# Performance work log

Measured on AMD Instinct MI355X. Metric: run time of the kernel, lower is better.

## Reference

```python
import jax, jax.numpy as jnp
import numpy as np

C_A = 768; C_S = 384; C_Z = 128; H = 16; D = C_A // H
B = 1; N = 4096; NQ = 32; NK = 128; NB = N // NQ
EPS = 1e-5


def _ln(x):
    # layernorm without learned affine (affine applied by caller where present)
    m = jnp.mean(x, axis=-1, keepdims=True)
    v = jnp.mean((x - m) ** 2, axis=-1, keepdims=True)
    return (x - m) * jax.lax.rsqrt(v + EPS)


def setup_inputs() -> dict:
    key = jax.random.key(0)
    ks = jax.random.split(key, 16)
    w = lambda k, shp: jax.random.normal(k, shp, dtype=jnp.float32) * 0.02
    return dict(
        a=jax.random.normal(ks[0], (B, N, C_A), jnp.float32),
        s=jax.random.normal(ks[1], (B, N, C_S), jnp.float32),
        z=jax.random.normal(ks[2], (B, NB, NQ, NK, C_Z), jnp.float32),
        adaln_gamma_s=jnp.ones((C_S,), jnp.float32),
        adaln_ws=w(ks[3], (C_S, C_A)),
        adaln_bs=jnp.zeros((C_A,), jnp.float32),
        adaln_wskip=w(ks[4], (C_S, C_A)),
        lnz_gamma=jnp.ones((C_Z,), jnp.float32),
        wz=w(ks[5], (C_Z, H)),
        wq=w(ks[6], (C_A, C_A)), bq=jnp.zeros((C_A,), jnp.float32),
        wk=w(ks[7], (C_A, C_A)),
        wv=w(ks[8], (C_A, C_A)),
        wg=w(ks[9], (C_A, C_A)), bg=jnp.ones((C_A,), jnp.float32),
        wo=w(ks[10], (C_A, C_A)), bo=jnp.zeros((C_A,), jnp.float32),
        w_last=w(ks[11], (C_S, C_A)),
        b_last=jnp.full((C_A,), -2.0, jnp.float32),  # biasinit = -2.0
        n_queries=NQ, n_keys=NK,
    )


def _forward(a, s, z, adaln_gamma_s, adaln_ws, adaln_bs, adaln_wskip,
             lnz_gamma, wz, wq, bq, wk, wv, wg, bg, wo, bo,
             w_last, b_last, n_queries, n_keys):
    Bq, Nq, _ = a.shape
    nb = Nq // n_queries
    # AdaptiveLayerNorm (AF3 Alg 26): a <- sigmoid(Lin(s_ln)) * LN(a) + LinNoBias(s_ln)
    s_ln = _ln(s) * adaln_gamma_s
    a_ln = jax.nn.sigmoid(s_ln @ adaln_ws + adaln_bs) * _ln(a) + s_ln @ adaln_wskip
    # pair bias: LN(z) (no offset) -> per-head bias, permuted to [B,H,nb,nq,nk]
    bias = (_ln(z) * lnz_gamma) @ wz                    # [B, nb, nq, nk, H]
    bias = jnp.transpose(bias, (0, 4, 1, 2, 3))          # [B, H, nb, nq, nk]
    # projections (q has bias; k/v no bias)
    q = (a_ln @ wq + bq).reshape(Bq, nb, n_queries, H, D)
    k = (a_ln @ wk).reshape(Bq, Nq, H, D)
    v = (a_ln @ wv).reshape(Bq, Nq, H, D)
    # local window: query block w covers [w*nq, (w+1)*nq); keys are nk centered on it
    start = jnp.arange(nb) * n_queries + n_queries // 2 - n_keys // 2
    kidx = start[:, None] + jnp.arange(n_keys)[None, :]  # [nb, nk]
    valid = (kidx >= 0) & (kidx < Nq)
    kidx = jnp.clip(kidx, 0, Nq - 1)
    k_loc = k[:, kidx]                                    # [B, nb, nk, H, D]
    v_loc = v[:, kidx]
    scale = 1.0 / float(np.sqrt(D))
    scores = jnp.einsum('bwqhd,bwkhd->bhwqk', q, k_loc) * scale + bias
    scores = jnp.where(valid[None, None, :, None, :], scores, -1e9)
    p = jax.nn.softmax(scores, axis=-1)
    o = jnp.einsum('bhwqk,bwkhd->bwqhd', p, v_loc).reshape(Bq, Nq, C_A)
    # gating, output projection, final sigmoid gate from raw s
    o = (jax.nn.sigmoid(a_ln @ wg + bg) * o) @ wo + bo
    return jax.nn.sigmoid(s @ w_last + b_last) * o


def reference(a, s, z, adaln_gamma_s, adaln_ws, adaln_bs, adaln_wskip,
              lnz_gamma, wz, wq, bq, wk, wv, wg, bg, wo, bo,
              w_last, b_last, n_queries, n_keys):
    return _forward(a, s, z, adaln_gamma_s, adaln_ws, adaln_bs, adaln_wskip,
                    lnz_gamma, wz, wq, bq, wk, wv, wg, bg, wo, bo,
                    w_last, b_last, n_queries, n_keys)
```

## Files before the change

### kernel.cpp

```cpp
#include <hip/hip_runtime.h>
#include <hip/hip_bf16.h>
#include <math.h>

#define N_TOK 4096
#define CA 768
#define CS 384
#define CZ 128
#define NHEAD 16
#define DH 48
#define NQW 32
#define NKW 128
#define NBLK 128
#define VT_W 4224

typedef __attribute__((ext_vector_type(8))) short short8;
typedef __attribute__((ext_vector_type(4))) float float4v;
typedef __attribute__((ext_vector_type(4))) unsigned short ushort4v;

__device__ __forceinline__ float sigmoidf_(float x){ return 1.0f/(1.0f+__expf(-x)); }

__device__ __forceinline__ unsigned short f2bf(float x){
  unsigned u = __float_as_uint(x);
  unsigned r = (u + 0x7FFFu + ((u>>16)&1u)) >> 16;
  return (unsigned short)r;
}
__device__ __forceinline__ float bf2f(unsigned short b){
  return __uint_as_float(((unsigned)b)<<16);
}
__device__ __forceinline__ short8 cvt8(const float* xv){
  union { short8 v; unsigned short u[8]; } H;
  #pragma unroll
  for (int j=0;j<8;j++) H.u[j] = f2bf(xv[j]);
  return H.v;
}
__device__ __forceinline__ short8 cvt8pk(const float* x){
  union { short8 v; unsigned u32[4]; } H;
  #pragma unroll
  for (int i=0;i<4;i++)
    asm("v_cvt_pk_bf16_f32 %0, %1, %2" : "=v"(H.u32[i]) : "v"(x[2*i]), "v"(x[2*i+1]));
  return H.v;
}

__device__ __forceinline__ void gload_lds16(const void* gsrc, void* ldst){
  __builtin_amdgcn_global_load_lds(
    (const __attribute__((address_space(1))) void*)gsrc,
    (__attribute__((address_space(3))) void*)ldst, 16, 0, 0);
}

__device__ __forceinline__ int xcd_swz(int wg, int nwg){
  int cpx = nwg >> 3;
  return (wg & 7)*cpx + (wg >> 3);
}

__global__ __launch_bounds__(256) void prep_kernel(
  const float* __restrict__ s, const float* __restrict__ adaln_gamma,
  unsigned short* __restrict__ s_ln_h, unsigned short* __restrict__ s_h,
  const float* __restrict__ a, float* __restrict__ a_n,
  const float* __restrict__ ws, const float* __restrict__ wskip,
  const float* __restrict__ wq, const float* __restrict__ wk,
  const float* __restrict__ wv, const float* __restrict__ wg,
  const float* __restrict__ wo, const float* __restrict__ wlast,
  unsigned short* __restrict__ Wt1, unsigned short* __restrict__ Wt2,
  unsigned short* __restrict__ Wt3, unsigned short* __restrict__ Wt4,
  const float* __restrict__ bq, const float* __restrict__ bg,
  float* __restrict__ biasq)
{
  __shared__ float tile[64][65];
  int bid = blockIdx.x;
  int tid = threadIdx.x;

  if (bid < 1024){
    int wave = tid>>6, lane = tid&63;
    int row = bid*4 + wave;
    const float* x = s + (size_t)row*CS;
    float v[6]; float sum=0.f, sq=0.f;
    #pragma unroll
    for (int i=0;i<6;i++){ v[i]=x[lane+64*i]; sum+=v[i]; sq+=v[i]*v[i]; }
    #pragma unroll
    for (int off=32; off; off>>=1){ sum+=__shfl_xor(sum,off); sq+=__shfl_xor(sq,off); }
    float m = sum*(1.f/CS);
    float var = sq*(1.f/CS)-m*m;
    float rs = rsqrtf(var+1e-5f);
    #pragma unroll
    for (int i=0;i<6;i++){
      int c = lane+64*i;
      s_ln_h[(size_t)row*CS+c] = f2bf((v[i]-m)*rs*adaln_gamma[c]);
      s_h[(size_t)row*CS+c]    = f2bf(v[i]);
    }
    return;
  }
  bid -= 1024;

  if (bid < 1024){
    int wave = tid>>6, lane = tid&63;
    int row = bid*4 + wave;
    const float* x = a + (size_t)row*CA;
    float v[12]; float sum=0.f, sq=0.f;
    #pragma unroll
    for (int i=0;i<12;i++){ v[i]=x[lane+64*i]; sum+=v[i]; sq+=v[i]*v[i]; }
    #pragma unroll
    for (int off=32; off; off>>=1){ sum+=__shfl_xor(sum,off); sq+=__shfl_xor(sq,off); }
    float m = sum*(1.f/CA);
    float var = sq*(1.f/CA)-m*m;
    float rs = rsqrtf(var+1e-5f);
    float* o = a_n + (size_t)row*CA;
    #pragma unroll
    for (int i=0;i<12;i++) o[lane+64*i] = (v[i]-m)*rs;
    return;
  }
  bid -= 1024;

  if (bid < 936){
    const float* src; unsigned short* dst; int K; int local;
    if      (bid < 72)  { src=ws;    dst=Wt1;                   K=CS; local=bid; }
    else if (bid < 144) { src=wskip; dst=Wt1 + (size_t)768*CS;  K=CS; local=bid-72; }
    else if (bid < 288) { src=wq;    dst=Wt2;                   K=CA; local=bid-144; }
    else if (bid < 432) { src=wk;    dst=Wt2 + (size_t)768*CA;  K=CA; local=bid-288; }
    else if (bid < 576) { src=wv;    dst=Wt2 + (size_t)1536*CA; K=CA; local=bid-432; }
    else if (bid < 720) { src=wg;    dst=Wt2 + (size_t)2304*CA; K=CA; local=bid-576; }
    else if (bid < 864) { src=wo;    dst=Wt3;                   K=CA; local=bid-720; }
    else                { src=wlast; dst=Wt4;                   K=CS; local=bid-864; }
    int ktiles = K/64;
    int kb = (local % ktiles)*64, nb = (local / ktiles)*64;
    int c = tid & 63, r0 = tid >> 6;
    #pragma unroll
    for (int i=0;i<16;i++){
      int r = r0 + 4*i;
      tile[r][c] = src[(size_t)(kb+r)*CA + nb + c];
    }
    __syncthreads();
    #pragma unroll
    for (int i=0;i<16;i++){
      int r = r0 + 4*i;
      dst[(size_t)(nb+r)*K + kb + c] = f2bf(tile[c][r]);
    }
    return;
  }
  bid -= 936;

  int i = bid*256 + tid;
  float v = 0.f;
  if (i < 768) v = bq[i];
  else if (i >= 2304) v = bg[i-2304];
  biasq[i] = v;
}

__global__ __launch_bounds__(128) void zbias_kernel(const float* __restrict__ z,
                                                    const float* __restrict__ gamma,
                                                    const float* __restrict__ wz,
                                                    unsigned short* __restrict__ bias3){
  __shared__ float zbuf[2][2][2048];
  int tid = threadIdx.x, wave = tid>>6, lane = tid&63;
  int lr = lane&15, quad = lane>>4;

  short8 bwh[4];
  float w1 = 0.f;
  #pragma unroll
  for (int ks=0;ks<4;ks++){
    float wv[8];
    #pragma unroll
    for (int j=0;j<8;j++){
      int k = ks*32 + quad*8 + j;
      wv[j] = wz[k*NHEAD + lr]*gamma[k];
      w1 += wv[j];
    }
    bwh[ks] = cvt8pk(wv);
  }
  w1 += __shfl_xor(w1, 16);
  w1 += __shfl_xor(w1, 32);

  size_t group = (size_t)blockIdx.x*2 + wave;
  const float* zg = z + group*(size_t)(NKW*CZ);
  unsigned short* outg = bias3 + group*2048;

  int rsub = lane>>5;
  int csw  = lane&31;
  auto stage = [&](int buf, int b){
    #pragma unroll
    for (int i=0;i<8;i++){
      int r  = 2*i + rsub;
      int gc = csw ^ (r & 7);
      gload_lds16(zg + (size_t)(b*16 + r)*CZ + gc*4, &zbuf[wave][buf][i*256]);
    }
  };

  stage(0, 0);
  int buf = 0;
  #pragma unroll 1
  for (int b=0; b<8; ++b){
    if (b < 7){
      stage(buf^1, b+1);
      asm volatile("s_waitcnt vmcnt(8)" ::: "memory");
    } else {
      asm volatile("s_waitcnt vmcnt(0)" ::: "memory");
    }
    __builtin_amdgcn_sched_barrier(0);

    const float* rowp = &zbuf[wave][buf][lr*128];
    int s = lr & 7;
    float4 p[8];
    #pragma unroll
    for (int ks=0;ks<4;ks++){
      int c0 = ks*8 + quad*2;
      p[ks*2]   = *(const float4*)(rowp + (size_t)((c0  )^s)*4);
      p[ks*2+1] = *(const float4*)(rowp + (size_t)((c0+1)^s)*4);
    }
    float sum=0.f, sq=0.f;
    #pragma unroll
    for (int t=0;t<8;t++){
      sum += p[t].x + p[t].y + p[t].z + p[t].w;
      sq  += p[t].x*p[t].x + p[t].y*p[t].y + p[t].z*p[t].z + p[t].w*p[t].w;
    }
    sum += __shfl_xor(sum,16); sum += __shfl_xor(sum,32);
    sq  += __shfl_xor(sq,16);  sq  += __shfl_xor(sq,32);
    float mean = sum*(1.f/CZ);
    float var  = sq*(1.f/CZ) - mean*mean;
    float rs = rsqrtf(var + 1e-5f);

    float4v c = (float4v){0.f,0.f,0.f,0.f};
    #pragma unroll
    for (int ks=0;ks<4;ks++){
      float xv[8];
      xv[0]=p[ks*2].x;   xv[1]=p[ks*2].y;   xv[2]=p[ks*2].z;   xv[3]=p[ks*2].w;
      xv[4]=p[ks*2+1].x; xv[5]=p[ks*2+1].y; xv[6]=p[ks*2+1].z; xv[7]=p[ks*2+1].w;
      c = __builtin_amdgcn_mfma_f32_16x16x32_bf16(cvt8pk(xv), bwh[ks], c, 0,0,0);
    }

    ushort4v o4;
    #pragma unroll
    for (int r=0;r<4;r++){
      int rrow = quad*4 + r;
      float m_r  = __shfl(mean, rrow);
      float rs_r = __shfl(rs, rrow);
      o4[r] = f2bf(rs_r*(c[r] - m_r*w1));
    }
    *(ushort4v*)(outg + lr*128 + b*16 + quad*4) = o4;
    buf ^= 1;
  }
}

__global__ __launch_bounds__(256) void adaln_gemm(
  const unsigned short* __restrict__ A, const unsigned short* __restrict__ Bt,
  const float* __restrict__ bs, const float* __restrict__ a_n,
  unsigned short* __restrict__ outh)
{
  __shared__ unsigned short Ash[128*32];
  __shared__ unsigned short B1sh[128*32];
  __shared__ unsigned short B2sh[128*32];

  int tid = threadIdx.x;
  int w = tid >> 6, lane = tid & 63;
  int lr = lane & 15, quad = lane >> 4;
  int wg = xcd_swz(blockIdx.y*gridDim.x + blockIdx.x, gridDim.x*gridDim.y);
  int bx = wg % gridDim.x, by = wg / gridDim.x;
  int m0 = by*128, n0 = bx*128;
  int mbase = (w&1)*64, nbase = (w>>1)*64;

  float4v acc1[4][4], acc2[4][4];
  #pragma unroll
  for (int i=0;i<4;i++)
    #pragma unroll
    for (int j=0;j<4;j++){
      acc1[i][j] = (float4v){0.f,0.f,0.f,0.f};
      acc2[i][j] = (float4v){0.f,0.f,0.f,0.f};
    }

  int grow = w*32 + (lane>>2);
  int gcol8 = (lane&3)*8;

  for (int k0=0; k0<CS; k0+=32){
    __syncthreads();
    #pragma unroll
    for (int i=0;i<2;i++){
      int rA = grow + i*16;
      gload_lds16(A  + (size_t)(m0 + rA)*CS + k0 + gcol8, &Ash[(w*32 + i*16)*32]);
      gload_lds16(Bt + (size_t)(n0 + rA)*CS + k0 + gcol8, &B1sh[(w*32 + i*16)*32]);
      gload_lds16(Bt + (size_t)(768 + n0 + rA)*CS + k0 + gcol8, &B2sh[(w*32 + i*16)*32]);
    }
    __syncthreads();

    short8 af[4], b1f[4], b2f[4];
    #pragma unroll
    for (int mi=0;mi<4;mi++)
      af[mi] = *(const short8*)&Ash[(mbase + mi*16 + lr)*32 + quad*8];
    #pragma unroll
    for (int ni=0;ni<4;ni++){
      b1f[ni] = *(const short8*)&B1sh[(nbase + ni*16 + lr)*32 + quad*8];
      b2f[ni] = *(const short8*)&B2sh[(nbase + ni*16 + lr)*32 + quad*8];
    }
    #pragma unroll
    for (int mi=0;mi<4;mi++)
      #pragma unroll
      for (int ni=0;ni<4;ni++){
        acc1[mi][ni] = __builtin_amdgcn_mfma_f32_16x16x32_bf16(af[mi], b1f[ni], acc1[mi][ni], 0,0,0);
        acc2[mi][ni] = __builtin_amdgcn_mfma_f32_16x16x32_bf16(af[mi], b2f[ni], acc2[mi][ni], 0,0,0);
      }
  }

  #pragma unroll
  for (int ni=0;ni<4;ni++){
    int col = n0 + nbase + ni*16 + lr;
    float bsv = bs[col];
    #pragma unroll
    for (int mi=0;mi<4;mi++){
      #pragma unroll
      for (int reg=0;reg<4;reg++){
        int row = m0 + mbase + mi*16 + quad*4 + reg;
        float v = sigmoidf_(acc1[mi][ni][reg] + bsv)*a_n[(size_t)row*CA + col] + acc2[mi][ni][reg];
        outh[(size_t)row*CA + col] = f2bf(v);
      }
    }
  }
}

template<int MODE>
__global__ __launch_bounds__(256) void gemm_bf16(
  const unsigned short* __restrict__ A1, const unsigned short* __restrict__ B1,
  const float* __restrict__ bias1, int K1,
  const unsigned short* __restrict__ A2, const unsigned short* __restrict__ B2,
  const float* __restrict__ bias2, int K2,
  void* __restrict__ outp, int M, int N)
{
  __shared__ unsigned short Ash[128*32];
  __shared__ unsigned short Bsh[128*32];

  int tid = threadIdx.x;
  int w = tid >> 6, lane = tid & 63;
  int lr = lane & 15, quad = lane >> 4;
  int wg = xcd_swz(blockIdx.y*gridDim.x + blockIdx.x, gridDim.x*gridDim.y);
  int bx = wg % gridDim.x, by = wg / gridDim.x;
  int m0 = by*128, n0 = bx*128;
  int mbase = (w&1)*64, nbase = (w>>1)*64;

  float4v acc1[4][4];
  float4v acc2[4][4];
  #pragma unroll
  for (int i=0;i<4;i++)
    #pragma unroll
    for (int j=0;j<4;j++){
      acc1[i][j] = (float4v){0.f,0.f,0.f,0.f};
      if constexpr (MODE == 3) acc2[i][j] = (float4v){0.f,0.f,0.f,0.f};
    }

  int grow = w*32 + (lane>>2);
  int gcol8 = (lane&3)*8;

  for (int k0=0; k0<K1; k0+=32){
    __syncthreads();
    #pragma unroll
    for (int i=0;i<2;i++){
      int rA = grow + i*16;
      gload_lds16(A1 + (size_t)(m0 + rA)*K1 + k0 + gcol8, &Ash[(w*32 + i*16)*32]);
      gload_lds16(B1 + (size_t)(n0 + rA)*K1 + k0 + gcol8, &Bsh[(w*32 + i*16)*32]);
    }
    __syncthreads();

    short8 af[4], bf[4];
    #pragma unroll
    for (int mi=0;mi<4;mi++)
      af[mi] = *(const short8*)&Ash[(mbase + mi*16 + lr)*32 + quad*8];
    #pragma unroll
    for (int ni=0;ni<4;ni++)
      bf[ni] = *(const short8*)&Bsh[(nbase + ni*16 + lr)*32 + quad*8];
    #pragma unroll
    for (int mi=0;mi<4;mi++)
      #pragma unroll
      for (int ni=0;ni<4;ni++)
        acc1[mi][ni] = __builtin_amdgcn_mfma_f32_16x16x32_bf16(af[mi], bf[ni], acc1[mi][ni], 0,0,0);
  }

  if constexpr (MODE == 3){
    for (int k0=0; k0<K2; k0+=32){
      __syncthreads();
      #pragma unroll
      for (int i=0;i<2;i++){
        int rA = grow + i*16;
        gload_lds16(A2 + (size_t)(m0 + rA)*K2 + k0 + gcol8, &Ash[(w*32 + i*16)*32]);
        gload_lds16(B2 + (size_t)(n0 + rA)*K2 + k0 + gcol8, &Bsh[(w*32 + i*16)*32]);
      }
      __syncthreads();

      short8 af[4], bf[4];
      #pragma unroll
      for (int mi=0;mi<4;mi++)
        af[mi] = *(const short8*)&Ash[(mbase + mi*16 + lr)*32 + quad*8];
      #pragma unroll
      for (int ni=0;ni<4;ni++)
        bf[ni] = *(const short8*)&Bsh[(nbase + ni*16 + lr)*32 + quad*8];
      #pragma unroll
      for (int mi=0;mi<4;mi++)
        #pragma unroll
        for (int ni=0;ni<4;ni++)
          acc2[mi][ni] = __builtin_amdgcn_mfma_f32_16x16x32_bf16(af[mi], bf[ni], acc2[mi][ni], 0,0,0);
    }
  }

  #pragma unroll
  for (int ni=0;ni<4;ni++){
    int col = n0 + nbase + ni*16 + lr;
    float bv1 = bias1 ? bias1[col] : 0.f;
    float bv2 = (MODE==3 && bias2) ? bias2[col] : 0.f;
    #pragma unroll
    for (int mi=0;mi<4;mi++){
      #pragma unroll
      for (int reg=0;reg<4;reg++){
        int row = m0 + mbase + mi*16 + quad*4 + reg;
        float x1 = acc1[mi][ni][reg] + bv1;
        if constexpr (MODE == 1)
          ((unsigned short*)outp)[(size_t)row*N + col] = f2bf(x1);
        else
          ((float*)outp)[(size_t)row*N + col] = sigmoidf_(acc2[mi][ni][reg] + bv2)*x1;
      }
    }
  }
}

__global__ __launch_bounds__(256) void vtrans_kernel(const unsigned short* __restrict__ qh,
                                                     unsigned short* __restrict__ Vt){
  __shared__ unsigned short tile[64][66];
  int t0 = blockIdx.x*64, c0 = blockIdx.y*64;
  int tid = threadIdx.x;
  int c = tid & 63, r0 = tid >> 6;
  #pragma unroll
  for (int i=0;i<16;i++){
    int r = r0 + 4*i;
    tile[r][c] = qh[(size_t)(t0+r)*3072 + 1536 + c0 + c];
  }
  if (t0 == 0){
    #pragma unroll
    for (int i=0;i<16;i++){
      int r = r0 + 4*i;
      Vt[(size_t)(c0+r)*VT_W + c] = 0;
    }
  } else if (t0 == N_TOK-64){
    #pragma unroll
    for (int i=0;i<16;i++){
      int r = r0 + 4*i;
      Vt[(size_t)(c0+r)*VT_W + 64 + N_TOK + c] = 0;
    }
  }
  __syncthreads();
  #pragma unroll
  for (int i=0;i<16;i++){
    int r = r0 + 4*i;
    Vt[(size_t)(c0+r)*VT_W + 64 + t0 + c] = tile[c][r];
  }
}

__global__ __launch_bounds__(256) void attn_kernel(
  const unsigned short* __restrict__ qh,
  const unsigned short* __restrict__ Vt,
  const unsigned short* __restrict__ bias3h,
  unsigned short* __restrict__ og)
{
  __shared__ unsigned short Pb[4][32*40];
  int tid = threadIdx.x, wave = tid>>6, lane = tid&63;
  int lr = lane&15, quad = lane>>4;
  int wg = xcd_swz(blockIdx.y*NBLK + blockIdx.x, NBLK*4);
  int w = wg % NBLK, hg = wg / NBLK;
  int h = hg*4 + wave;
  int start = w*NQW - 48;
  const float scale = 0.14433756729740643f;

  short8 zero8 = {0,0,0,0,0,0,0,0};

  short8 aq[2][2];
  #pragma unroll
  for (int mt=0;mt<2;mt++){
    int row = w*NQW + mt*16 + lr;
    const unsigned short* qp = qh + (size_t)row*3072 + h*DH;
    aq[mt][0] = *(const short8*)(qp + quad*8);
    aq[mt][1] = (quad<2) ? *(const short8*)(qp + 32 + quad*8) : zero8;
  }

  float4v c[2][8];
  #pragma unroll
  for (int mt=0;mt<2;mt++)
    #pragma unroll
    for (int nt=0;nt<8;nt++) c[mt][nt] = (float4v){0.f,0.f,0.f,0.f};

  #pragma unroll 2
  for (int nt=0;nt<8;nt++){
    int krc = min(max(start + nt*16 + lr,0),N_TOK-1);
    const unsigned short* kp = qh + (size_t)krc*3072 + 768 + h*DH;
    short8 bk0 = *(const short8*)(kp + quad*8);
    short8 bk1 = (quad<2) ? *(const short8*)(kp + 32 + quad*8) : zero8;
    #pragma unroll
    for (int mt=0;mt<2;mt++){
      c[mt][nt] = __builtin_amdgcn_mfma_f32_16x16x32_bf16(aq[mt][0], bk0, c[mt][nt], 0,0,0);
      c[mt][nt] = __builtin_amdgcn_mfma_f32_16x16x32_bf16(aq[mt][1], bk1, c[mt][nt], 0,0,0);
    }
  }

  short8 vb[2][2][3];
  #pragma unroll
  for (int c2=0;c2<2;c2++)
    #pragma unroll
    for (int ks=0;ks<2;ks++)
      #pragma unroll
      for (int no=0;no<3;no++){
        int col = h*DH + no*16 + lr;
        vb[c2][ks][no] = *(const short8*)(Vt + (size_t)col*VT_W + 64 + start + c2*64 + ks*32 + quad*8);
      }

  float rmax[2][4], rsum[2][4];
  #pragma unroll
  for (int mt=0;mt<2;mt++)
    #pragma unroll
    for (int r=0;r<4;r++){ rmax[mt][r] = -3.0e38f; rsum[mt][r] = 0.f; }

  #pragma unroll
  for (int nt=0;nt<8;nt++){
    int key = start + nt*16 + lr;
    bool valid = (key>=0) && (key<N_TOK);
    #pragma unroll
    for (int mt=0;mt<2;mt++){
      #pragma unroll
      for (int r=0;r<4;r++){
        int q = mt*16 + quad*4 + r;
        float bv = bf2f(bias3h[(((size_t)(w*NQW+q))*NHEAD + h)*128 + nt*16 + lr]);
        float v = valid ? (c[mt][nt][r]*scale + bv) : -1e9f;
        c[mt][nt][r] = v;
        rmax[mt][r] = fmaxf(rmax[mt][r], v);
      }
    }
  }
  #pragma unroll
  for (int mt=0;mt<2;mt++)
    #pragma unroll
    for (int r=0;r<4;r++){
      float m = rmax[mt][r];
      m = fmaxf(m, __shfl_xor(m,1)); m = fmaxf(m, __shfl_xor(m,2));
      m = fmaxf(m, __shfl_xor(m,4)); m = fmaxf(m, __shfl_xor(m,8));
      rmax[mt][r] = m;
    }
  #pragma unroll
  for (int nt=0;nt<8;nt++)
    #pragma unroll
    for (int mt=0;mt<2;mt++)
      #pragma unroll
      for (int r=0;r<4;r++){
        float e = __expf(c[mt][nt][r] - rmax[mt][r]);
        c[mt][nt][r] = e;
        rsum[mt][r] += e;
      }
  #pragma unroll
  for (int mt=0;mt<2;mt++)
    #pragma unroll
    for (int r=0;r<4;r++){
      float sv = rsum[mt][r];
      sv += __shfl_xor(sv,1); sv += __shfl_xor(sv,2);
      sv += __shfl_xor(sv,4); sv += __shfl_xor(sv,8);
      rsum[mt][r] = 1.f/sv;
    }

  unsigned short* ph = &Pb[wave][0];
  float4v o[2][3];
  #pragma unroll
  for (int mt=0;mt<2;mt++)
    #pragma unroll
    for (int no=0;no<3;no++) o[mt][no] = (float4v){0.f,0.f,0.f,0.f};

  #pragma unroll
  for (int c2=0;c2<2;c2++){
    #pragma unroll
    for (int ks=0;ks<2;ks++){
      int ntb = c2*4 + ks*2;
      #pragma unroll
      for (int t=0;t<2;t++){
        int nt = ntb + t;
        #pragma unroll
        for (int mt=0;mt<2;mt++){
          #pragma unroll
          for (int r=0;r<4;r++){
            int q = mt*16 + quad*4 + r;
            ph[q*40 + t*16 + lr] = f2bf(c[mt][nt][r]*rsum[mt][r]);
          }
        }
      }
      short8 pa[2];
      #pragma unroll
      for (int mt=0;mt<2;mt++)
        pa[mt] = *(const short8*)&ph[(mt*16+lr)*40 + quad*8];
      #pragma unroll
      for (int no=0;no<3;no++){
        #pragma unroll
        for (int mt=0;mt<2;mt++)
          o[mt][no] = __builtin_amdgcn_mfma_f32_16x16x32_bf16(pa[mt], vb[c2][ks][no], o[mt][no], 0,0,0);
      }
    }
  }

  #pragma unroll
  for (int mt=0;mt<2;mt++){
    #pragma unroll
    for (int no=0;no<3;no++){
      int d = no*16 + lr;
      #pragma unroll
      for (int r=0;r<4;r++){
        int q = mt*16 + quad*4 + r;
        size_t grow = (size_t)(w*NQW + q);
        float g = bf2f(qh[grow*3072 + 2304 + h*DH + d]);
        og[grow*CA + h*DH + d] = f2bf(o[mt][no][r] * sigmoidf_(g));
      }
    }
  }
}

extern "C" void kernel_launch(void* const* d_in, const int* in_sizes, int n_in,
                              void* d_out, int out_size, void* d_ws, size_t ws_size,
                              hipStream_t stream)
{
  const float* a            = (const float*)d_in[0];
  const float* s            = (const float*)d_in[1];
  const float* z            = (const float*)d_in[2];
  const float* adaln_gamma  = (const float*)d_in[3];
  const float* adaln_ws     = (const float*)d_in[4];
  const float* adaln_bs     = (const float*)d_in[5];
  const float* adaln_wskip  = (const float*)d_in[6];
  const float* lnz_gamma    = (const float*)d_in[7];
  const float* wz           = (const float*)d_in[8];
  const float* wq           = (const float*)d_in[9];
  const float* bq           = (const float*)d_in[10];
  const float* wk           = (const float*)d_in[11];
  const float* wv           = (const float*)d_in[12];
  const float* wg           = (const float*)d_in[13];
  const float* bg           = (const float*)d_in[14];
  const float* wo           = (const float*)d_in[15];
  const float* bo           = (const float*)d_in[16];
  const float* w_last       = (const float*)d_in[17];
  const float* b_last       = (const float*)d_in[18];
  float* out = (float*)d_out;

  char* base = (char*)d_ws;
  size_t off = 0;
  auto alloc = [&](size_t bytes)->char*{ char* p = base + off; off += (bytes + 255) & ~(size_t)255; return p; };

  unsigned short* s_ln_h = (unsigned short*)alloc((size_t)N_TOK*CS*2);
  unsigned short* s_h    = (unsigned short*)alloc((size_t)N_TOK*CS*2);
  float*          a_n    = (float*)alloc((size_t)N_TOK*CA*4);
  unsigned short* a_ln_h = (unsigned short*)alloc((size_t)N_TOK*CA*2);
  unsigned short* og_h   = (unsigned short*)alloc((size_t)N_TOK*CA*2);
  unsigned short* Wt1    = (unsigned short*)alloc((size_t)1536*CS*2);
  unsigned short* Wt2    = (unsigned short*)alloc((size_t)3072*CA*2);
  unsigned short* Wt3    = (unsigned short*)alloc((size_t)CA*CA*2);
  unsigned short* Wt4    = (unsigned short*)alloc((size_t)CA*CS*2);
  unsigned short* bias3h = (unsigned short*)alloc((size_t)N_TOK*NHEAD*NKW*2);
  unsigned short* qkvg_h = (unsigned short*)alloc((size_t)N_TOK*3072*2);
  unsigned short* Vt     = (unsigned short*)alloc((size_t)CA*VT_W*2);
  float*          biasq  = (float*)alloc((size_t)3072*4);

  prep_kernel<<<dim3(1024+1024+936+12), 256, 0, stream>>>(
      s, adaln_gamma, s_ln_h, s_h, a, a_n,
      adaln_ws, adaln_wskip, wq, wk, wv, wg, wo, w_last,
      Wt1, Wt2, Wt3, Wt4, bq, bg, biasq);

  zbias_kernel<<<dim3(N_TOK/2), 128, 0, stream>>>(z, lnz_gamma, wz, bias3h);

  adaln_gemm<<<dim3(CA/128, N_TOK/128), 256, 0, stream>>>(s_ln_h, Wt1, adaln_bs, a_n, a_ln_h);

  gemm_bf16<1><<<dim3(3072/128, N_TOK/128), 256, 0, stream>>>(
      a_ln_h, Wt2, biasq, CA, nullptr, nullptr, nullptr, 0, qkvg_h, N_TOK, 3072);

  vtrans_kernel<<<dim3(N_TOK/64, CA/64), 256, 0, stream>>>(qkvg_h, Vt);

  attn_kernel<<<dim3(NBLK, 4), 256, 0, stream>>>(qkvg_h, Vt, bias3h, og_h);

  gemm_bf16<3><<<dim3(CA/128, N_TOK/128), 256, 0, stream>>>(
      og_h, Wt3, bo, CA, s_h, Wt4, b_last, CS, out, N_TOK, CA);
}
```

Before: 234.8 us.

## Fuse z-bias into prep kernel and stage V in LDS inside attention

The pair-bias LayerNorm+projection work moves into the prep kernel as an extra range of blocks, with four waves per block, so one launch is saved. The separate V transpose kernel and its global Vt buffer are removed. Instead, each attention block loads its 128-key by 4-head V window into swizzled LDS and gathers V operands per lane with scalar LDS reads. The attention kernel also drops the XCD swizzle and stops unrolling the PV loops. In exchange it adds a __syncthreads, more LDS traffic and element-wise gathers in the inner loop.

After: 232.8 us. About the same (-0.9%).

```diff
diff --git a/kernel.cpp b/kernel.cpp
--- a/kernel.cpp
+++ b/kernel.cpp
@@ -11,7 +11,6 @@
 #define NQW 32
 #define NKW 128
 #define NBLK 128
-#define VT_W 4224
 
 typedef __attribute__((ext_vector_type(8))) short short8;
 typedef __attribute__((ext_vector_type(4))) float float4v;
@@ -52,7 +51,9 @@
   return (wg & 7)*cpx + (wg >> 3);
 }
 
-__global__ __launch_bounds__(256) void prep_kernel(
+__global__ __launch_bounds__(256) void prep_zbias_kernel(
+  const float* __restrict__ z, const float* __restrict__ lnz_gamma,
+  const float* __restrict__ wz, unsigned short* __restrict__ bias3,
   const float* __restrict__ s, const float* __restrict__ adaln_gamma,
   unsigned short* __restrict__ s_ln_h, unsigned short* __restrict__ s_h,
   const float* __restrict__ a, float* __restrict__ a_n,
@@ -65,9 +66,105 @@
   const float* __restrict__ bq, const float* __restrict__ bg,
   float* __restrict__ biasq)
 {
-  __shared__ float tile[64][65];
+  union PZ {
+    float tile[64][65];
+    float zbuf[4][2][2048];
+  };
+  __shared__ PZ sm;
   int bid = blockIdx.x;
   int tid = threadIdx.x;
+
+  if (bid < 1024){
+    int wave = tid>>6, lane = tid&63;
+    int lr = lane&15, quad = lane>>4;
+
+    short8 bwh[4];
+    float w1 = 0.f;
+    #pragma unroll
+    for (int ks=0;ks<4;ks++){
+      float wv_[8];
+      #pragma unroll
+      for (int j=0;j<8;j++){
+        int k = ks*32 + quad*8 + j;
+        wv_[j] = wz[k*NHEAD + lr]*lnz_gamma[k];
+        w1 += wv_[j];
+      }
+      bwh[ks] = cvt8pk(wv_);
+    }
+    w1 += __shfl_xor(w1, 16);
+    w1 += __shfl_xor(w1, 32);
+
+    size_t group = (size_t)bid*4 + wave;
+    const float* zg = z + group*(size_t)(NKW*CZ);
+    unsigned short* outg = bias3 + group*2048;
+
+    int rsub = lane>>5;
+    int csw  = lane&31;
+    auto stage = [&](int buf, int b){
+      #pragma unroll
+      for (int i=0;i<8;i++){
+        int r  = 2*i + rsub;
+        int gc = csw ^ (r & 7);
+        gload_lds16(zg + (size_t)(b*16 + r)*CZ + gc*4, &sm.zbuf[wave][buf][i*256]);
+      }
+    };
+
+    stage(0, 0);
+    int buf = 0;
+    #pragma unroll 1
+    for (int b=0; b<8; ++b){
+      if (b < 7){
+        stage(buf^1, b+1);
+        asm volatile("s_waitcnt vmcnt(8)" ::: "memory");
+      } else {
+        asm volatile("s_waitcnt vmcnt(0)" ::: "memory");
+      }
+      __builtin_amdgcn_sched_barrier(0);
+
+      const float* rowp = &sm.zbuf[wave][buf][lr*128];
+      int sswz = lr & 7;
+      float4 p[8];
+      #pragma unroll
+      for (int ks=0;ks<4;ks++){
+        int c0 = ks*8 + quad*2;
+        p[ks*2]   = *(const float4*)(rowp + (size_t)((c0  )^sswz)*4);
+        p[ks*2+1] = *(const float4*)(rowp + (size_t)((c0+1)^sswz)*4);
+      }
+      float sum=0.f, sq=0.f;
+      #pragma unroll
+      for (int t=0;t<8;t++){
+        sum += p[t].x + p[t].y + p[t].z + p[t].w;
+        sq  += p[t].x*p[t].x + p[t].y*p[t].y + p[t].z*p[t].z + p[t].w*p[t].w;
+      }
+      sum += __shfl_xor(sum,16); sum += __shfl_xor(sum,32);
+      sq  += __shfl_xor(sq,16);  sq  += __shfl_xor(sq,32);
+      float mean = sum*(1.f/CZ);
+      float var  = sq*(1.f/CZ) - mean*mean;
+      float rs = rsqrtf(var + 1e-5f);
+
+      float4v c = (float4v){0.f,0.f,0.f,0.f};
+      #pragma unroll
+      for (int ks=0;ks<4;ks++){
+        float xv[8];
+        xv[0]=p[ks*2].x;   xv[1]=p[ks*2].y;   xv[2]=p[ks*2].z;   xv[3]=p[ks*2].w;
+        xv[4]=p[ks*2+1].x; xv[5]=p[ks*2+1].y; xv[6]=p[ks*2+1].z; xv[7]=p[ks*2+1].w;
+        c = __builtin_amdgcn_mfma_f32_16x16x32_bf16(cvt8pk(xv), bwh[ks], c, 0,0,0);
+      }
+
+      ushort4v o4;
+      #pragma unroll
+      for (int r=0;r<4;r++){
+        int rrow = quad*4 + r;
+        float m_r  = __shfl(mean, rrow);
+        float rs_r = __shfl(rs, rrow);
+        o4[r] = f2bf(rs_r*(c[r] - m_r*w1));
+      }
+      *(ushort4v*)(outg + lr*128 + b*16 + quad*4) = o4;
+      buf ^= 1;
+    }
+    return;
+  }
+  bid -= 1024;
 
   if (bid < 1024){
     int wave = tid>>6, lane = tid&63;
@@ -126,13 +223,13 @@
     #pragma unroll
     for (int i=0;i<16;i++){
       int r = r0 + 4*i;
-      tile[r][c] = src[(size_t)(kb+r)*CA + nb + c];
+      sm.tile[r][c] = src[(size_t)(kb+r)*CA + nb + c];
     }
     __syncthreads();
     #pragma unroll
     for (int i=0;i<16;i++){
       int r = r0 + 4*i;
-      dst[(size_t)(nb+r)*K + kb + c] = f2bf(tile[c][r]);
+      dst[(size_t)(nb+r)*K + kb + c] = f2bf(sm.tile[c][r]);
     }
     return;
   }
@@ -143,100 +240,6 @@
   if (i < 768) v = bq[i];
   else if (i >= 2304) v = bg[i-2304];
   biasq[i] = v;
-}
-
-__global__ __launch_bounds__(128) void zbias_kernel(const float* __restrict__ z,
-                                                    const float* __restrict__ gamma,
-                                                    const float* __restrict__ wz,
-                                                    unsigned short* __restrict__ bias3){
-  __shared__ float zbuf[2][2][2048];
-  int tid = threadIdx.x, wave = tid>>6, lane = tid&63;
-  int lr = lane&15, quad = lane>>4;
-
-  short8 bwh[4];
-  float w1 = 0.f;
-  #pragma unroll
-  for (int ks=0;ks<4;ks++){
-    float wv[8];
-    #pragma unroll
-    for (int j=0;j<8;j++){
-      int k = ks*32 + quad*8 + j;
-      wv[j] = wz[k*NHEAD + lr]*gamma[k];
-      w1 += wv[j];
-    }
-    bwh[ks] = cvt8pk(wv);
-  }
-  w1 += __shfl_xor(w1, 16);
-  w1 += __shfl_xor(w1, 32);
-
-  size_t group = (size_t)blockIdx.x*2 + wave;
-  const float* zg = z + group*(size_t)(NKW*CZ);
-  unsigned short* outg = bias3 + group*2048;
-
-  int rsub = lane>>5;
-  int csw  = lane&31;
-  auto stage = [&](int buf, int b){
-    #pragma unroll
-    for (int i=0;i<8;i++){
-      int r  = 2*i + rsub;
-      int gc = csw ^ (r & 7);
-      gload_lds16(zg + (size_t)(b*16 + r)*CZ + gc*4, &zbuf[wave][buf][i*256]);
-    }
-  };
-
-  stage(0, 0);
-  int buf = 0;
-  #pragma unroll 1
-  for (int b=0; b<8; ++b){
-    if (b < 7){
-      stage(buf^1, b+1);
-      asm volatile("s_waitcnt vmcnt(8)" ::: "memory");
-    } else {
-      asm volatile("s_waitcnt vmcnt(0)" ::: "memory");
-    }
-    __builtin_amdgcn_sched_barrier(0);
-
-    const float* rowp = &zbuf[wave][buf][lr*128];
-    int s = lr & 7;
-    float4 p[8];
-    #pragma unroll
-    for (int ks=0;ks<4;ks++){
-      int c0 = ks*8 + quad*2;
-      p[ks*2]   = *(const float4*)(rowp + (size_t)((c0  )^s)*4);
-      p[ks*2+1] = *(const float4*)(rowp + (size_t)((c0+1)^s)*4);
-    }
-    float sum=0.f, sq=0.f;
-    #pragma unroll
-    for (int t=0;t<8;t++){
-      sum += p[t].x + p[t].y + p[t].z + p[t].w;
-      sq  += p[t].x*p[t].x + p[t].y*p[t].y + p[t].z*p[t].z + p[t].w*p[t].w;
-    }
-    sum += __shfl_xor(sum,16); sum += __shfl_xor(sum,32);
-    sq  += __shfl_xor(sq,16);  sq  += __shfl_xor(sq,32);
-    float mean = sum*(1.f/CZ);
-    float var  = sq*(1.f/CZ) - mean*mean;
-    float rs = rsqrtf(var + 1e-5f);
-
-    float4v c = (float4v){0.f,0.f,0.f,0.f};
-    #pragma unroll
-    for (int ks=0;ks<4;ks++){
-      float xv[8];
-      xv[0]=p[ks*2].x;   xv[1]=p[ks*2].y;   xv[2]=p[ks*2].z;   xv[3]=p[ks*2].w;
-      xv[4]=p[ks*2+1].x; xv[5]=p[ks*2+1].y; xv[6]=p[ks*2+1].z; xv[7]=p[ks*2+1].w;
-      c = __builtin_amdgcn_mfma_f32_16x16x32_bf16(cvt8pk(xv), bwh[ks], c, 0,0,0);
-    }
-
-    ushort4v o4;
-    #pragma unroll
-    for (int r=0;r<4;r++){
-      int rrow = quad*4 + r;
-      float m_r  = __shfl(mean, rrow);
-      float rs_r = __shfl(rs, rrow);
-      o4[r] = f2bf(rs_r*(c[r] - m_r*w1));
-    }
-    *(ushort4v*)(outg + lr*128 + b*16 + quad*4) = o4;
-    buf ^= 1;
-  }
 }
 
 __global__ __launch_bounds__(256) void adaln_gemm(
@@ -415,52 +418,31 @@
   }
 }
 
-__global__ __launch_bounds__(256) void vtrans_kernel(const unsigned short* __restrict__ qh,
-                                                     unsigned short* __restrict__ Vt){
-  __shared__ unsigned short tile[64][66];
-  int t0 = blockIdx.x*64, c0 = blockIdx.y*64;
-  int tid = threadIdx.x;
-  int c = tid & 63, r0 = tid >> 6;
-  #pragma unroll
-  for (int i=0;i<16;i++){
-    int r = r0 + 4*i;
-    tile[r][c] = qh[(size_t)(t0+r)*3072 + 1536 + c0 + c];
-  }
-  if (t0 == 0){
-    #pragma unroll
-    for (int i=0;i<16;i++){
-      int r = r0 + 4*i;
-      Vt[(size_t)(c0+r)*VT_W + c] = 0;
-    }
-  } else if (t0 == N_TOK-64){
-    #pragma unroll
-    for (int i=0;i<16;i++){
-      int r = r0 + 4*i;
-      Vt[(size_t)(c0+r)*VT_W + 64 + N_TOK + c] = 0;
-    }
-  }
-  __syncthreads();
-  #pragma unroll
-  for (int i=0;i<16;i++){
-    int r = r0 + 4*i;
-    Vt[(size_t)(c0+r)*VT_W + 64 + t0 + c] = tile[c][r];
-  }
-}
-
 __global__ __launch_bounds__(256) void attn_kernel(
   const unsigned short* __restrict__ qh,
-  const unsigned short* __restrict__ Vt,
   const unsigned short* __restrict__ bias3h,
   unsigned short* __restrict__ og)
 {
+  __shared__ unsigned short Vs[128*192];
   __shared__ unsigned short Pb[4][32*40];
   int tid = threadIdx.x, wave = tid>>6, lane = tid&63;
   int lr = lane&15, quad = lane>>4;
-  int wg = xcd_swz(blockIdx.y*NBLK + blockIdx.x, NBLK*4);
-  int w = wg % NBLK, hg = wg / NBLK;
-  int h = hg*4 + wave;
+  int w = blockIdx.x, h = blockIdx.y*4 + wave;
   int start = w*NQW - 48;
   const float scale = 0.14433756729740643f;
+
+  {
+    int hbase = blockIdx.y*4*DH;
+    #pragma unroll
+    for (int it=0; it<12; ++it){
+      int c = it*256 + tid;
+      int key = c/24, cc = c - key*24;
+      int kr = min(max(start+key,0),N_TOK-1);
+      short8 v = *(const short8*)&qh[(size_t)kr*3072 + 1536 + hbase + cc*8];
+      int cs = cc ^ (((key>>3)&3)*2);
+      *(short8*)&Vs[key*192 + cs*8] = v;
+    }
+  }
 
   short8 zero8 = {0,0,0,0,0,0,0,0};
 
@@ -492,17 +474,6 @@
     }
   }
 
-  short8 vb[2][2][3];
-  #pragma unroll
-  for (int c2=0;c2<2;c2++)
-    #pragma unroll
-    for (int ks=0;ks<2;ks++)
-      #pragma unroll
-      for (int no=0;no<3;no++){
-        int col = h*DH + no*16 + lr;
-        vb[c2][ks][no] = *(const short8*)(Vt + (size_t)col*VT_W + 64 + start + c2*64 + ks*32 + quad*8);
-      }
-
   float rmax[2][4], rsum[2][4];
   #pragma unroll
   for (int mt=0;mt<2;mt++)
@@ -554,6 +525,8 @@
       rsum[mt][r] = 1.f/sv;
     }
 
+  __syncthreads();
+
   unsigned short* ph = &Pb[wave][0];
   float4v o[2][3];
   #pragma unroll
@@ -561,9 +534,9 @@
     #pragma unroll
     for (int no=0;no<3;no++) o[mt][no] = (float4v){0.f,0.f,0.f,0.f};
 
-  #pragma unroll
+  #pragma unroll 1
   for (int c2=0;c2<2;c2++){
-    #pragma unroll
+    #pragma unroll 1
     for (int ks=0;ks<2;ks++){
       int ntb = c2*4 + ks*2;
       #pragma unroll
@@ -584,9 +557,18 @@
         pa[mt] = *(const short8*)&ph[(mt*16+lr)*40 + quad*8];
       #pragma unroll
       for (int no=0;no<3;no++){
+        union { short8 v; unsigned short u[8]; } V;
+        int col = wave*DH + no*16 + lr;
+        int chunk = col >> 3;
+        int cs = (chunk ^ (quad*2))*8 + (col & 7);
+        #pragma unroll
+        for (int j=0;j<8;j++){
+          int key = c2*64 + ks*32 + quad*8 + j;
+          V.u[j] = Vs[key*192 + cs];
+        }
         #pragma unroll
         for (int mt=0;mt<2;mt++)
-          o[mt][no] = __builtin_amdgcn_mfma_f32_16x16x32_bf16(pa[mt], vb[c2][ks][no], o[mt][no], 0,0,0);
+          o[mt][no] = __builtin_amdgcn_mfma_f32_16x16x32_bf16(pa[mt], V.v, o[mt][no], 0,0,0);
       }
     }
   }
@@ -647,24 +629,20 @@
   unsigned short* Wt4    = (unsigned short*)alloc((size_t)CA*CS*2);
   unsigned short* bias3h = (unsigned short*)alloc((size_t)N_TOK*NHEAD*NKW*2);
   unsigned short* qkvg_h = (unsigned short*)alloc((size_t)N_TOK*3072*2);
-  unsigned short* Vt     = (unsigned short*)alloc((size_t)CA*VT_W*2);
   float*          biasq  = (float*)alloc((size_t)3072*4);
 
-  prep_kernel<<<dim3(1024+1024+936+12), 256, 0, stream>>>(
+  prep_zbias_kernel<<<dim3(1024+1024+1024+936+12), 256, 0, stream>>>(
+      z, lnz_gamma, wz, bias3h,
       s, adaln_gamma, s_ln_h, s_h, a, a_n,
       adaln_ws, adaln_wskip, wq, wk, wv, wg, wo, w_last,
       Wt1, Wt2, Wt3, Wt4, bq, bg, biasq);
 
-  zbias_kernel<<<dim3(N_TOK/2), 128, 0, stream>>>(z, lnz_gamma, wz, bias3h);
-
   adaln_gemm<<<dim3(CA/128, N_TOK/128), 256, 0, stream>>>(s_ln_h, Wt1, adaln_bs, a_n, a_ln_h);
 
   gemm_bf16<1><<<dim3(3072/128, N_TOK/128), 256, 0, stream>>>(
       a_ln_h, Wt2, biasq, CA, nullptr, nullptr, nullptr, 0, qkvg_h, N_TOK, 3072);
 
-  vtrans_kernel<<<dim3(N_TOK/64, CA/64), 256, 0, stream>>>(qkvg_h, Vt);
-
-  attn_kernel<<<dim3(NBLK, 4), 256, 0, stream>>>(qkvg_h, Vt, bias3h, og_h);
+  attn_kernel<<<dim3(NBLK, 4), 256, 0, stream>>>(qkvg_h, bias3h, og_h);
 
   gemm_bf16<3><<<dim3(CA/128, N_TOK/128), 256, 0, stream>>>(
       og_h, Wt3, bo, CA, s_h, Wt4, b_last, CS, out, N_TOK, CA);
```
